# Performance work log

Hardware: AMD Instinct MI355X
Metric: run time of the kernel (lower is better)

Reference implementation:

```python
import jax, jax.numpy as jnp
import numpy as np

B, T, N, C, H, K = 32, 12, 512, 2, 64, 3
P = C + H  # 66, GCN input feature dim


def _xavier(key, fan_in, fan_out):
    std = (2.0 / (fan_in + fan_out)) ** 0.5
    return jax.random.normal(key, (fan_in, fan_out), dtype=jnp.float32) * std


def setup_inputs() -> dict:
    key = jax.random.key(0)
    k1, k2, k3, k4 = jax.random.split(key, 4)
    # scale adjacency so K-hop aggregation stays O(1) in magnitude
    G = jax.random.normal(k1, (K, N, N), dtype=jnp.float32) * (1.0 / np.sqrt(N))
    x_seq = jax.random.normal(k2, (B, T, N, C), dtype=jnp.float32)
    init_h = jnp.zeros((B, N, H), dtype=jnp.float32)
    W_gate = _xavier(k3, K * P, 2 * H)
    b_gate = jnp.zeros((2 * H,), dtype=jnp.float32)
    W_update = _xavier(k4, K * P, H)
    b_update = jnp.zeros((H,), dtype=jnp.float32)
    return {"G": G, "x_seq": x_seq, "init_h": init_h,
            "W_gate": W_gate, "b_gate": b_gate,
            "W_update": W_update, "b_update": b_update}


def _gcn(G, x, W, b):
    # x: [B, N, P]; G: [K, N, N] -> support_cat: [B, N, K*P] (k-major, matching torch cat order)
    Bq, Nq, Pq = x.shape
    sup = jnp.einsum('kij,bjp->bikp', G, x).reshape(Bq, Nq, -1)
    return sup @ W + b


def _cell(G, x, h, Wg, bg, Wu, bu):
    combined = jnp.concatenate([x, h], axis=-1)             # [B,N,C+H]
    zr = jax.nn.sigmoid(_gcn(G, combined, Wg, bg))           # [B,N,2H]
    z, r = zr[..., :H], zr[..., H:]
    candidate = jnp.concatenate([x, r * h], axis=-1)
    hc = jnp.tanh(_gcn(G, candidate, Wu, bu))
    return (1.0 - z) * h + z * hc


def reference(G, x_seq, init_h, W_gate, b_gate, W_update, b_update):
    # scan over time (sequential GRU state dependency)
    xs = jnp.swapaxes(x_seq, 0, 1)  # [T,B,N,C]

    def step(h, x_t):
        h2 = _cell(G, x_t, h, W_gate, b_gate, W_update, b_update)
        return h2, None

    h_last, _ = jax.lax.scan(step, init_h, xs)
    return h_last  # [B,N,H] — last hidden state of the (single) layer
```

## Files before the change

kernel.cpp:

```cpp
#include <hip/hip_runtime.h>
#include <hip/hip_bf16.h>
#include <cmath>

#define NN 512
#define BB 32
#define HH 64
#define TT 12
#define KS 3

#define OFF_GHI   0
#define OFF_GPK   786432
#define OFF_XTH   1572864
#define OFF_SX    1966080
#define OFF_HHI   3145728
#define OFF_HLO   3670016
#define OFF_RHHI  4194304
#define OFF_Z     4718592
#define OFF_WHGH  6291456
#define OFF_WHGL  6304256
#define OFF_WHUH  6317056
#define OFF_WHUL  6323456
#define OFF_WXG   6329856
#define OFF_WXU   6330624

typedef __attribute__((ext_vector_type(8))) short v8s;
typedef __attribute__((ext_vector_type(4))) float f32x4;
typedef __attribute__((ext_vector_type(4))) unsigned short u16x4;

__device__ __forceinline__ unsigned short f2bf(float f) {
  union { __hip_bfloat16 h; unsigned short u; } x;
  x.h = __float2bfloat16(f);
  return x.u;
}
__device__ __forceinline__ float bf2f(unsigned short u) {
  union { unsigned short u; __hip_bfloat16 h; } x;
  x.u = u;
  return __bfloat162float(x.h);
}

__device__ __forceinline__ int swz64(int j, int key) {
  return (j & ~63) | ((((j >> 3) & 7) ^ key) << 3) | (j & 7);
}

__device__ __forceinline__ void gl_lds16(const unsigned short* g, short* l) {
  __builtin_amdgcn_global_load_lds(
      (const __attribute__((address_space(1))) void*)g,
      (__attribute__((address_space(3))) void*)l, 16, 0, 0);
}

__device__ __forceinline__ float fast_tanh(float x) {
  float e = __expf(2.f * x);
  return 1.f - 2.f / (e + 1.f);
}

__global__ __launch_bounds__(256) void prep_all(
    const float* __restrict__ G, const float* __restrict__ x_seq,
    const float* __restrict__ init_h, const float* __restrict__ Wg,
    const float* __restrict__ Wu,
    unsigned short* __restrict__ Ghi, unsigned short* __restrict__ Gpk,
    unsigned short* __restrict__ Xh,
    unsigned short* __restrict__ Hhi, unsigned short* __restrict__ Hlo,
    unsigned short* __restrict__ Whgh, unsigned short* __restrict__ Whgl,
    unsigned short* __restrict__ Whuh, unsigned short* __restrict__ Whul,
    float* __restrict__ Wxg, float* __restrict__ Wxu) {
  int idx = blockIdx.x * 256 + threadIdx.x;
  if (idx < 786432) {
    int j = idx & 511;
    int i = (idx >> 9) & 511;
    Ghi[(size_t)(idx >> 9) * 512 + swz64(j, i & 7)] = f2bf(G[idx]);
  } else if (idx < 884736) {
    int t = idx - 786432;
    int L = t & 63;
    int frag = t >> 6;
    int m = frag % 3;
    int kf = (frag / 3) & 1;
    int j0 = (frag / 6) & 7;
    int i0w = frag / 48;
    int w = i0w & 3, i0 = i0w >> 2;
    int R = w * 48 + m * 16 + (L & 15);
    int ksec = R >> 6;
    int i = i0 * 64 + (R & 63);
    int jb = j0 * 64 + kf * 32 + (L >> 4) * 8;
    unsigned short* dst = Gpk + (size_t)frag * 512 + L * 8;
#pragma unroll
    for (int e = 0; e < 8; ++e) dst[e] = f2bf(G[((size_t)ksec * NN + i) * NN + jb + e]);
  } else if (idx < 1277952) {
    int t2 = idx - 884736;
    int j = t2 & 511;
    int col = t2 >> 9;
    int t = col >> 6;
    int b = (col & 63) >> 1;
    int c = col & 1;
    float v = x_seq[((size_t)(b * TT + t) * NN + j) * 2 + c];
    Xh[(size_t)col * 512 + swz64(j, col & 7)] = f2bf(v);
  } else if (idx < 2326528) {
    int t2 = idx - 1277952;
    int i = t2 & 511;
    int col = t2 >> 9;
    int b = col >> 6;
    int p = col & 63;
    float h = init_h[((size_t)b * NN + i) * HH + p];
    unsigned short hi = f2bf(h);
    size_t pos = (size_t)col * 512 + swz64(i, col & 7);
    Hhi[pos] = hi;
    Hlo[pos] = f2bf(h - bf2f(hi));
  } else if (idx < 2364544) {
    int j2 = idx - 2326528;
    if (j2 < 24576) {
      int o = j2 & 127, kq = j2 >> 7;
      int k = kq >> 6, q = kq & 63;
      float v = Wg[(size_t)(k * 66 + 2 + q) * 128 + o];
      unsigned short hi = f2bf(v);
      Whgh[o * 200 + kq] = hi;
      Whgl[o * 200 + kq] = f2bf(v - bf2f(hi));
    } else if (j2 < 36864) {
      int j = j2 - 24576;
      int o = j & 63, kq = j >> 6;
      int k = kq >> 6, q = kq & 63;
      float v = Wu[(size_t)(k * 66 + 2 + q) * 64 + o];
      unsigned short hi = f2bf(v);
      Whuh[o * 200 + kq] = hi;
      Whul[o * 200 + kq] = f2bf(v - bf2f(hi));
    } else if (j2 < 37632) {
      int j = j2 - 36864;
      int o = j & 127, kc = j >> 7;
      Wxg[kc * 128 + o] = Wg[(size_t)((kc >> 1) * 66 + (kc & 1)) * 128 + o];
    } else {
      int j = j2 - 37632;
      int o = j & 63, kc = j >> 6;
      Wxu[kc * 64 + o] = Wu[(size_t)((kc >> 1) * 66 + (kc & 1)) * 64 + o];
    }
  }
}

__global__ __launch_bounds__(256) void gemm_sx(const unsigned short* __restrict__ Ghi,
                                               const unsigned short* __restrict__ Xh,
                                               float* __restrict__ Sx2) {
  __shared__ __align__(16) short sA[64 * 64];
  __shared__ __align__(16) short sB[64 * 64];
  int tid = threadIdx.x;
  int L = tid & 63, w = tid >> 6;
  int wm = (w >> 1) * 32, wn = (w & 1) * 32;
  int i0 = blockIdx.y * 64;
  int c0 = blockIdx.x * 64;
  f32x4 acc[2][2];
#pragma unroll
  for (int m = 0; m < 2; ++m)
#pragma unroll
    for (int n = 0; n < 2; ++n) acc[m][n] = (f32x4)(0.f);

  for (int j0 = 0; j0 < 512; j0 += 64) {
    __syncthreads();
#pragma unroll
    for (int u = 0; u < 2; ++u) {
      int r = w * 16 + u * 8;
      gl_lds16(Ghi + (size_t)(i0 + r + (L >> 3)) * 512 + j0 + (L & 7) * 8, sA + r * 64);
      gl_lds16(Xh + (size_t)(c0 + r + (L >> 3)) * 512 + j0 + (L & 7) * 8, sB + r * 64);
    }
    __syncthreads();
#pragma unroll
    for (int kf = 0; kf < 2; ++kf) {
      int kog = kf * 4 + (L >> 4);
      v8s af[2], bf[2];
#pragma unroll
      for (int m = 0; m < 2; ++m) {
        int row = wm + m * 16 + (L & 15);
        af[m] = *(const v8s*)(sA + row * 64 + ((kog ^ (row & 7)) << 3));
      }
#pragma unroll
      for (int n = 0; n < 2; ++n) {
        int row = wn + n * 16 + (L & 15);
        bf[n] = *(const v8s*)(sB + row * 64 + ((kog ^ (row & 7)) << 3));
      }
#pragma unroll
      for (int m = 0; m < 2; ++m)
#pragma unroll
        for (int n = 0; n < 2; ++n)
          acc[m][n] = __builtin_amdgcn_mfma_f32_16x16x32_bf16(af[m], bf[n], acc[m][n], 0, 0, 0);
    }
  }
#pragma unroll
  for (int m = 0; m < 2; ++m)
#pragma unroll
    for (int r = 0; r < 4; ++r)
#pragma unroll
      for (int n = 0; n < 2; ++n)
        Sx2[(size_t)(i0 + wm + m * 16 + (L >> 4) * 4 + r) * 768 + c0 + wn + n * 16 + (L & 15)] =
            acc[m][n][r];
}

template <int GATE>
__global__ __launch_bounds__(512, 2) void fused_step(
    const unsigned short* __restrict__ Gpk,
    const unsigned short* __restrict__ Bhi,
    const float* __restrict__ Sx2,
    const unsigned short* __restrict__ Whi,
    const unsigned short* __restrict__ Wlo,
    const float* __restrict__ Wx,
    const float* __restrict__ bias,
    const unsigned short* __restrict__ Hr_hi,
    const unsigned short* __restrict__ Hr_lo,
    unsigned short* __restrict__ Ohi,
    unsigned short* __restrict__ Olo,
    unsigned short* __restrict__ Z,
    float* __restrict__ out, int t) {
  constexpr int O = GATE ? 128 : 64;
  constexpr int NF = GATE ? 4 : 2;
  __shared__ __align__(16) char smem[67584];
  short* sBh = (short*)smem;
  short* sS  = (short*)smem;
  float* sSx = (float*)(smem + 65536);

  int tid = threadIdx.x;
  int L = tid & 63, w = tid >> 6;
  int wm = w & 3, wn = w >> 2;
  int bid = blockIdx.x;
  int c = bid & 7, local = bid >> 3;
  int p = c >> 1, hc = c & 1;
  int b = p * 8 + (local >> 2);
  int i0t = hc * 4 + (local & 3);
  int i0 = i0t * 64;
  int bcol = b * 64;
  const unsigned short* Ap = Gpk + (size_t)(i0t * 4 + wm) * 48 * 512;

#pragma unroll
  for (int u = 0; u < 8; ++u) {
    int col = w * 8 + u;
    gl_lds16(Bhi + (size_t)(bcol + col) * 512 + L * 8, sBh + col * 512);
  }
  for (int e = tid; e < 384; e += 512) {
    int il = e / 6, kc = e % 6;
    sSx[e] = Sx2[(size_t)((kc >> 1) * 512 + i0 + il) * 768 + t * 64 + b * 2 + (kc & 1)];
  }
  __syncthreads();

  f32x4 acc[3][2];
#pragma unroll
  for (int m = 0; m < 3; ++m)
#pragma unroll
    for (int n = 0; n < 2; ++n) acc[m][n] = (f32x4)(0.f);
#pragma unroll
  for (int it = 0; it < 8; ++it) {
    v8s ah[2][3];
#pragma unroll
    for (int kf = 0; kf < 2; ++kf)
#pragma unroll
      for (int m = 0; m < 3; ++m)
        ah[kf][m] = *(const v8s*)(Ap + (size_t)((it * 2 + kf) * 3 + m) * 512 + L * 8);
#pragma unroll
    for (int kf = 0; kf < 2; ++kf) {
      int jj = it * 64 + kf * 32 + (L >> 4) * 8;
      v8s bh[2];
#pragma unroll
      for (int n = 0; n < 2; ++n) {
        int col = wn * 32 + n * 16 + (L & 15);
        int off = col * 512 + ((jj & ~63) | (((((jj >> 3) & 7) ^ (col & 7))) << 3));
        bh[n] = *(const v8s*)(sBh + off);
      }
#pragma unroll
      for (int m = 0; m < 3; ++m)
#pragma unroll
        for (int n = 0; n < 2; ++n)
          acc[m][n] = __builtin_amdgcn_mfma_f32_16x16x32_bf16(ah[kf][m], bh[n], acc[m][n], 0, 0, 0);
    }
  }
  __syncthreads();

#pragma unroll
  for (int m = 0; m < 3; ++m)
#pragma unroll
    for (int n = 0; n < 2; ++n)
#pragma unroll
      for (int r = 0; r < 4; ++r) {
        int R = wm * 48 + m * 16 + (L >> 4) * 4 + r;
        int il = R & 63, kk = R >> 6;
        int pp = wn * 32 + n * 16 + (L & 15);
        float v = acc[m][n][r];
        unsigned short hi = f2bf(v);
        sS[il * 408 + kk * 64 + pp] = (short)hi;
        sS[il * 408 + 200 + kk * 64 + pp] = (short)f2bf(v - bf2f(hi));
      }
  __syncthreads();

  int me = w & 3, oh = w >> 2;
  f32x4 acc2[NF];
#pragma unroll
  for (int n = 0; n < NF; ++n) acc2[n] = (f32x4)(0.f);
#pragma unroll
  for (int s = 0; s < 3; ++s) {
    const unsigned short* Wsrc = (s < 2) ? Whi : Wlo;
    int abase = (s == 1) ? 200 : 0;
#pragma unroll
    for (int f = 0; f < 6; ++f) {
      int k0 = f * 32 + (L >> 4) * 8;
      v8s af2 = *(const v8s*)(sS + (me * 16 + (L & 15)) * 408 + abase + k0);
#pragma unroll
      for (int n = 0; n < NF; ++n) {
        v8s bf2 = *(const v8s*)(Wsrc + (size_t)(oh * (O / 2) + n * 16 + (L & 15)) * 200 + k0);
        acc2[n] = __builtin_amdgcn_mfma_f32_16x16x32_bf16(af2, bf2, acc2[n], 0, 0, 0);
      }
    }
  }

#pragma unroll
  for (int n = 0; n < NF; ++n) {
    int o = oh * (O / 2) + n * 16 + (L & 15);
    int il0 = me * 16 + (L >> 4) * 4;
    float vals[4];
#pragma unroll
    for (int r = 0; r < 4; ++r) {
      float v = acc2[n][r] + bias[o];
#pragma unroll
      for (int kc = 0; kc < 6; ++kc) v += sSx[(il0 + r) * 6 + kc] * Wx[kc * O + o];
      vals[r] = v;
    }
    if (GATE) {
      float sg[4];
#pragma unroll
      for (int r = 0; r < 4; ++r) sg[r] = 1.f / (1.f + __expf(-vals[r]));
      if (oh == 0) {
#pragma unroll
        for (int r = 0; r < 4; ++r)
          Z[((size_t)b * 512 + i0 + il0 + r) * 64 + o] = f2bf(sg[r]);
      } else {
        int col = bcol + (o - 64);
        size_t cb = (size_t)col * 512 + i0 + (((il0 >> 3) ^ (col & 7)) << 3) + (il0 & 7);
        u16x4 h4 = *(const u16x4*)(Hr_hi + cb);
        u16x4 l4 = *(const u16x4*)(Hr_lo + cb);
        u16x4 oh4;
#pragma unroll
        for (int r = 0; r < 4; ++r) {
          float h = bf2f(h4[r]) + bf2f(l4[r]);
          oh4[r] = f2bf(sg[r] * h);
        }
        *(u16x4*)(Ohi + cb) = oh4;
      }
    } else {
      int col = bcol + o;
      size_t cb = (size_t)col * 512 + i0 + (((il0 >> 3) ^ (col & 7)) << 3) + (il0 & 7);
      u16x4 h4 = *(const u16x4*)(Hr_hi + cb);
      u16x4 l4 = *(const u16x4*)(Hr_lo + cb);
      u16x4 oh4, ol4;
#pragma unroll
      for (int r = 0; r < 4; ++r) {
        float hc2 = fast_tanh(vals[r]);
        float z = bf2f(Z[((size_t)b * 512 + i0 + il0 + r) * 64 + o]);
        float h = bf2f(h4[r]) + bf2f(l4[r]);
        float hn = (1.f - z) * h + z * hc2;
        unsigned short hi = f2bf(hn);
        oh4[r] = hi;
        ol4[r] = f2bf(hn - bf2f(hi));
        if (t == TT - 1) out[((size_t)b * 512 + i0 + il0 + r) * 64 + o] = hn;
      }
      *(u16x4*)(Ohi + cb) = oh4;
      *(u16x4*)(Olo + cb) = ol4;
    }
  }
}

extern "C" void kernel_launch(void* const* d_in, const int* in_sizes, int n_in,
                              void* d_out, int out_size, void* d_ws, size_t ws_size,
                              hipStream_t stream) {
  const float* G      = (const float*)d_in[0];
  const float* x_seq  = (const float*)d_in[1];
  const float* init_h = (const float*)d_in[2];
  const float* Wg     = (const float*)d_in[3];
  const float* bg     = (const float*)d_in[4];
  const float* Wu     = (const float*)d_in[5];
  const float* bu     = (const float*)d_in[6];
  float* out = (float*)d_out;
  float* ws = (float*)d_ws;

  unsigned short* GHI  = (unsigned short*)(ws + OFF_GHI);
  unsigned short* GPK  = (unsigned short*)(ws + OFF_GPK);
  unsigned short* Xh   = (unsigned short*)(ws + OFF_XTH);
  float* Sx2           = ws + OFF_SX;
  unsigned short* Hhi  = (unsigned short*)(ws + OFF_HHI);
  unsigned short* Hlo  = (unsigned short*)(ws + OFF_HLO);
  unsigned short* RHhi = (unsigned short*)(ws + OFF_RHHI);
  unsigned short* Z    = (unsigned short*)(ws + OFF_Z);
  unsigned short* Whgh = (unsigned short*)(ws + OFF_WHGH);
  unsigned short* Whgl = (unsigned short*)(ws + OFF_WHGL);
  unsigned short* Whuh = (unsigned short*)(ws + OFF_WHUH);
  unsigned short* Whul = (unsigned short*)(ws + OFF_WHUL);
  float* Wxg           = ws + OFF_WXG;
  float* Wxu           = ws + OFF_WXU;

  prep_all<<<9237, 256, 0, stream>>>(G, x_seq, init_h, Wg, Wu, GHI, GPK, Xh,
                                     Hhi, Hlo, Whgh, Whgl, Whuh, Whul, Wxg, Wxu);
  gemm_sx<<<dim3(12, 24), 256, 0, stream>>>(GHI, Xh, Sx2);

  for (int t = 0; t < TT; ++t) {
    fused_step<1><<<256, 512, 0, stream>>>(GPK, Hhi, Sx2, Whgh, Whgl, Wxg, bg,
                                           Hhi, Hlo, RHhi, RHhi, Z, out, t);
    fused_step<0><<<256, 512, 0, stream>>>(GPK, RHhi, Sx2, Whuh, Whul, Wxu, bu,
                                           Hhi, Hlo, Hhi, Hlo, Z, out, t);
  }
}
```

Measured before the change: 361.4 us.

## Replace per-step kernel launches with persistent kernel using per-batch group barriers

The 24 per-timestep launches of the gate and update kernels become one persistent kernel. Each block claims a slot on its own XCC via an atomic counter, so the 8 blocks of a batch share an XCC and synchronize through a lightweight per-batch group barrier instead of kernel boundaries. The z gate is kept in shared memory rather than round-tripped through global memory. This removes launch overhead and global Z traffic, but it relies on all 256 blocks being co-resident and on exactly 32 blocks landing on each XCC. The spin barrier has a timeout break, so a scheduling mismatch could give silently wrong results instead of a hang.

Result: slower. 1.263 ms (+249.6%).

```diff
diff --git a/kernel.cpp b/kernel.cpp
--- a/kernel.cpp
+++ b/kernel.cpp
@@ -15,7 +15,7 @@
 #define OFF_HHI   3145728
 #define OFF_HLO   3670016
 #define OFF_RHHI  4194304
-#define OFF_Z     4718592
+#define OFF_BAR   4718592
 #define OFF_WHGH  6291456
 #define OFF_WHGL  6304256
 #define OFF_WHUH  6317056
@@ -189,171 +189,230 @@
             acc[m][n][r];
 }
 
-template <int GATE>
-__global__ __launch_bounds__(512, 2) void fused_step(
+__device__ __forceinline__ void groupbar(unsigned int* gb) {
+  __syncthreads();
+  if (threadIdx.x == 0) {
+    __builtin_amdgcn_fence(__ATOMIC_RELEASE, "agent");
+    unsigned int g = __hip_atomic_load(gb + 1, __ATOMIC_RELAXED, __HIP_MEMORY_SCOPE_AGENT);
+    unsigned int old =
+        __hip_atomic_fetch_add(gb, 1u, __ATOMIC_RELEASE, __HIP_MEMORY_SCOPE_AGENT);
+    if (old == 7u) {
+      __hip_atomic_store(gb, 0u, __ATOMIC_RELAXED, __HIP_MEMORY_SCOPE_AGENT);
+      __hip_atomic_store(gb + 1, g + 1u, __ATOMIC_RELEASE, __HIP_MEMORY_SCOPE_AGENT);
+    } else {
+      int sp = 0;
+      while (__hip_atomic_load(gb + 1, __ATOMIC_ACQUIRE, __HIP_MEMORY_SCOPE_AGENT) == g) {
+        __builtin_amdgcn_s_sleep(2);
+        if (++sp > (1 << 24)) break;
+      }
+    }
+    __builtin_amdgcn_fence(__ATOMIC_ACQUIRE, "agent");
+  }
+  __syncthreads();
+}
+
+__global__ __launch_bounds__(512, 2) void persist(
     const unsigned short* __restrict__ Gpk,
-    const unsigned short* __restrict__ Bhi,
+    unsigned short* __restrict__ Hhi, unsigned short* __restrict__ Hlo,
+    unsigned short* __restrict__ RHhi,
     const float* __restrict__ Sx2,
-    const unsigned short* __restrict__ Whi,
-    const unsigned short* __restrict__ Wlo,
-    const float* __restrict__ Wx,
-    const float* __restrict__ bias,
-    const unsigned short* __restrict__ Hr_hi,
-    const unsigned short* __restrict__ Hr_lo,
-    unsigned short* __restrict__ Ohi,
-    unsigned short* __restrict__ Olo,
-    unsigned short* __restrict__ Z,
-    float* __restrict__ out, int t) {
-  constexpr int O = GATE ? 128 : 64;
-  constexpr int NF = GATE ? 4 : 2;
-  __shared__ __align__(16) char smem[67584];
+    const unsigned short* __restrict__ Whgh, const unsigned short* __restrict__ Whgl,
+    const float* __restrict__ Wxg, const float* __restrict__ bg,
+    const unsigned short* __restrict__ Whuh, const unsigned short* __restrict__ Whul,
+    const float* __restrict__ Wxu, const float* __restrict__ bu,
+    float* __restrict__ out, unsigned int* __restrict__ bar) {
+  __shared__ __align__(16) char smem[83456];
+  __shared__ unsigned int sSlot;
   short* sBh = (short*)smem;
   short* sS  = (short*)smem;
   float* sSx = (float*)(smem + 65536);
+  float* sZ  = (float*)(smem + 67072);
 
   int tid = threadIdx.x;
   int L = tid & 63, w = tid >> 6;
   int wm = w & 3, wn = w >> 2;
-  int bid = blockIdx.x;
-  int c = bid & 7, local = bid >> 3;
-  int p = c >> 1, hc = c & 1;
-  int b = p * 8 + (local >> 2);
-  int i0t = hc * 4 + (local & 3);
+
+  unsigned int xcc;
+  asm volatile("s_getreg_b32 %0, hwreg(HW_REG_XCC_ID)" : "=s"(xcc));
+  xcc &= 7u;
+  if (tid == 0) {
+    unsigned int s =
+        __hip_atomic_fetch_add(bar + xcc, 1u, __ATOMIC_RELAXED, __HIP_MEMORY_SCOPE_AGENT) & 31u;
+    sSlot = xcc * 32u + s;
+  }
+  __syncthreads();
+  unsigned int slot = sSlot;
+  int b = (int)(slot >> 3);
+  int i0t = (int)(slot & 7u);
   int i0 = i0t * 64;
   int bcol = b * 64;
+  unsigned int* gb = bar + 8 + b * 2;
   const unsigned short* Ap = Gpk + (size_t)(i0t * 4 + wm) * 48 * 512;
 
-#pragma unroll
-  for (int u = 0; u < 8; ++u) {
-    int col = w * 8 + u;
-    gl_lds16(Bhi + (size_t)(bcol + col) * 512 + L * 8, sBh + col * 512);
-  }
-  for (int e = tid; e < 384; e += 512) {
-    int il = e / 6, kc = e % 6;
-    sSx[e] = Sx2[(size_t)((kc >> 1) * 512 + i0 + il) * 768 + t * 64 + b * 2 + (kc & 1)];
-  }
-  __syncthreads();
-
-  f32x4 acc[3][2];
-#pragma unroll
-  for (int m = 0; m < 3; ++m)
-#pragma unroll
-    for (int n = 0; n < 2; ++n) acc[m][n] = (f32x4)(0.f);
-#pragma unroll
-  for (int it = 0; it < 8; ++it) {
-    v8s ah[2][3];
-#pragma unroll
-    for (int kf = 0; kf < 2; ++kf)
+  for (int t = 0; t < TT; ++t) {
+#pragma unroll 1
+    for (int ph = 0; ph < 2; ++ph) {
+      const int GATE = (ph == 0);
+      const unsigned short* Bsrc = GATE ? Hhi : RHhi;
+
+#pragma unroll
+      for (int u = 0; u < 8; ++u) {
+        int col = w * 8 + u;
+        gl_lds16(Bsrc + (size_t)(bcol + col) * 512 + L * 8, sBh + col * 512);
+      }
+      if (GATE) {
+        for (int e = tid; e < 384; e += 512) {
+          int il = e / 6, kc = e % 6;
+          sSx[e] = Sx2[(size_t)((kc >> 1) * 512 + i0 + il) * 768 + t * 64 + b * 2 + (kc & 1)];
+        }
+      }
+      __syncthreads();
+
+      f32x4 acc[3][2];
 #pragma unroll
       for (int m = 0; m < 3; ++m)
-        ah[kf][m] = *(const v8s*)(Ap + (size_t)((it * 2 + kf) * 3 + m) * 512 + L * 8);
-#pragma unroll
-    for (int kf = 0; kf < 2; ++kf) {
-      int jj = it * 64 + kf * 32 + (L >> 4) * 8;
-      v8s bh[2];
-#pragma unroll
-      for (int n = 0; n < 2; ++n) {
-        int col = wn * 32 + n * 16 + (L & 15);
-        int off = col * 512 + ((jj & ~63) | (((((jj >> 3) & 7) ^ (col & 7))) << 3));
-        bh[n] = *(const v8s*)(sBh + off);
-      }
+#pragma unroll
+        for (int n = 0; n < 2; ++n) acc[m][n] = (f32x4)(0.f);
+#pragma unroll
+      for (int it = 0; it < 8; ++it) {
+        v8s ah[2][3];
+#pragma unroll
+        for (int kf = 0; kf < 2; ++kf)
+#pragma unroll
+          for (int m = 0; m < 3; ++m)
+            ah[kf][m] = *(const v8s*)(Ap + (size_t)((it * 2 + kf) * 3 + m) * 512 + L * 8);
+#pragma unroll
+        for (int kf = 0; kf < 2; ++kf) {
+          int jj = it * 64 + kf * 32 + (L >> 4) * 8;
+          v8s bh[2];
+#pragma unroll
+          for (int n = 0; n < 2; ++n) {
+            int col = wn * 32 + n * 16 + (L & 15);
+            int off = col * 512 + ((jj & ~63) | (((((jj >> 3) & 7) ^ (col & 7))) << 3));
+            bh[n] = *(const v8s*)(sBh + off);
+          }
+#pragma unroll
+          for (int m = 0; m < 3; ++m)
+#pragma unroll
+            for (int n = 0; n < 2; ++n)
+              acc[m][n] =
+                  __builtin_amdgcn_mfma_f32_16x16x32_bf16(ah[kf][m], bh[n], acc[m][n], 0, 0, 0);
+        }
+      }
+      __syncthreads();
+
 #pragma unroll
       for (int m = 0; m < 3; ++m)
 #pragma unroll
         for (int n = 0; n < 2; ++n)
-          acc[m][n] = __builtin_amdgcn_mfma_f32_16x16x32_bf16(ah[kf][m], bh[n], acc[m][n], 0, 0, 0);
-    }
-  }
-  __syncthreads();
-
-#pragma unroll
-  for (int m = 0; m < 3; ++m)
-#pragma unroll
-    for (int n = 0; n < 2; ++n)
-#pragma unroll
-      for (int r = 0; r < 4; ++r) {
-        int R = wm * 48 + m * 16 + (L >> 4) * 4 + r;
-        int il = R & 63, kk = R >> 6;
-        int pp = wn * 32 + n * 16 + (L & 15);
-        float v = acc[m][n][r];
-        unsigned short hi = f2bf(v);
-        sS[il * 408 + kk * 64 + pp] = (short)hi;
-        sS[il * 408 + 200 + kk * 64 + pp] = (short)f2bf(v - bf2f(hi));
-      }
-  __syncthreads();
-
-  int me = w & 3, oh = w >> 2;
-  f32x4 acc2[NF];
-#pragma unroll
-  for (int n = 0; n < NF; ++n) acc2[n] = (f32x4)(0.f);
-#pragma unroll
-  for (int s = 0; s < 3; ++s) {
-    const unsigned short* Wsrc = (s < 2) ? Whi : Wlo;
-    int abase = (s == 1) ? 200 : 0;
-#pragma unroll
-    for (int f = 0; f < 6; ++f) {
-      int k0 = f * 32 + (L >> 4) * 8;
-      v8s af2 = *(const v8s*)(sS + (me * 16 + (L & 15)) * 408 + abase + k0);
-#pragma unroll
-      for (int n = 0; n < NF; ++n) {
-        v8s bf2 = *(const v8s*)(Wsrc + (size_t)(oh * (O / 2) + n * 16 + (L & 15)) * 200 + k0);
-        acc2[n] = __builtin_amdgcn_mfma_f32_16x16x32_bf16(af2, bf2, acc2[n], 0, 0, 0);
-      }
-    }
-  }
-
-#pragma unroll
-  for (int n = 0; n < NF; ++n) {
-    int o = oh * (O / 2) + n * 16 + (L & 15);
-    int il0 = me * 16 + (L >> 4) * 4;
-    float vals[4];
-#pragma unroll
-    for (int r = 0; r < 4; ++r) {
-      float v = acc2[n][r] + bias[o];
-#pragma unroll
-      for (int kc = 0; kc < 6; ++kc) v += sSx[(il0 + r) * 6 + kc] * Wx[kc * O + o];
-      vals[r] = v;
-    }
-    if (GATE) {
-      float sg[4];
-#pragma unroll
-      for (int r = 0; r < 4; ++r) sg[r] = 1.f / (1.f + __expf(-vals[r]));
-      if (oh == 0) {
-#pragma unroll
-        for (int r = 0; r < 4; ++r)
-          Z[((size_t)b * 512 + i0 + il0 + r) * 64 + o] = f2bf(sg[r]);
+#pragma unroll
+          for (int r = 0; r < 4; ++r) {
+            int R = wm * 48 + m * 16 + (L >> 4) * 4 + r;
+            int il = R & 63, kk = R >> 6;
+            int pp = wn * 32 + n * 16 + (L & 15);
+            float v = acc[m][n][r];
+            unsigned short hi = f2bf(v);
+            sS[il * 408 + kk * 64 + pp] = (short)hi;
+            sS[il * 408 + 200 + kk * 64 + pp] = (short)f2bf(v - bf2f(hi));
+          }
+      __syncthreads();
+
+      int me = w & 3, oh = w >> 2;
+      if (GATE) {
+        f32x4 acc2[4];
+#pragma unroll
+        for (int n = 0; n < 4; ++n) acc2[n] = (f32x4)(0.f);
+#pragma unroll
+        for (int s = 0; s < 3; ++s) {
+          const unsigned short* Wsrc = (s < 2) ? Whgh : Whgl;
+          int abase = (s == 1) ? 200 : 0;
+#pragma unroll
+          for (int f = 0; f < 6; ++f) {
+            int k0 = f * 32 + (L >> 4) * 8;
+            v8s af2 = *(const v8s*)(sS + (me * 16 + (L & 15)) * 408 + abase + k0);
+#pragma unroll
+            for (int n = 0; n < 4; ++n) {
+              v8s bf2 = *(const v8s*)(Wsrc + (size_t)(oh * 64 + n * 16 + (L & 15)) * 200 + k0);
+              acc2[n] = __builtin_amdgcn_mfma_f32_16x16x32_bf16(af2, bf2, acc2[n], 0, 0, 0);
+            }
+          }
+        }
+#pragma unroll
+        for (int n = 0; n < 4; ++n) {
+          int o = oh * 64 + n * 16 + (L & 15);
+          int il0 = me * 16 + (L >> 4) * 4;
+          float sg[4];
+#pragma unroll
+          for (int r = 0; r < 4; ++r) {
+            float v = acc2[n][r] + bg[o];
+#pragma unroll
+            for (int kc = 0; kc < 6; ++kc) v += sSx[(il0 + r) * 6 + kc] * Wxg[kc * 128 + o];
+            sg[r] = 1.f / (1.f + __expf(-v));
+          }
+          if (oh == 0) {
+#pragma unroll
+            for (int r = 0; r < 4; ++r) sZ[(il0 + r) * 64 + o] = sg[r];
+          } else {
+            int col = bcol + (o - 64);
+            size_t cb = (size_t)col * 512 + i0 + (((il0 >> 3) ^ (col & 7)) << 3) + (il0 & 7);
+            u16x4 h4 = *(const u16x4*)(Hhi + cb);
+            u16x4 l4 = *(const u16x4*)(Hlo + cb);
+            u16x4 oh4;
+#pragma unroll
+            for (int r = 0; r < 4; ++r) {
+              float h = bf2f(h4[r]) + bf2f(l4[r]);
+              oh4[r] = f2bf(sg[r] * h);
+            }
+            *(u16x4*)(RHhi + cb) = oh4;
+          }
+        }
       } else {
-        int col = bcol + (o - 64);
-        size_t cb = (size_t)col * 512 + i0 + (((il0 >> 3) ^ (col & 7)) << 3) + (il0 & 7);
-        u16x4 h4 = *(const u16x4*)(Hr_hi + cb);
-        u16x4 l4 = *(const u16x4*)(Hr_lo + cb);
-        u16x4 oh4;
-#pragma unroll
-        for (int r = 0; r < 4; ++r) {
-          float h = bf2f(h4[r]) + bf2f(l4[r]);
-          oh4[r] = f2bf(sg[r] * h);
-        }
-        *(u16x4*)(Ohi + cb) = oh4;
-      }
-    } else {
-      int col = bcol + o;
-      size_t cb = (size_t)col * 512 + i0 + (((il0 >> 3) ^ (col & 7)) << 3) + (il0 & 7);
-      u16x4 h4 = *(const u16x4*)(Hr_hi + cb);
-      u16x4 l4 = *(const u16x4*)(Hr_lo + cb);
-      u16x4 oh4, ol4;
-#pragma unroll
-      for (int r = 0; r < 4; ++r) {
-        float hc2 = fast_tanh(vals[r]);
-        float z = bf2f(Z[((size_t)b * 512 + i0 + il0 + r) * 64 + o]);
-        float h = bf2f(h4[r]) + bf2f(l4[r]);
-        float hn = (1.f - z) * h + z * hc2;
-        unsigned short hi = f2bf(hn);
-        oh4[r] = hi;
-        ol4[r] = f2bf(hn - bf2f(hi));
-        if (t == TT - 1) out[((size_t)b * 512 + i0 + il0 + r) * 64 + o] = hn;
-      }
-      *(u16x4*)(Ohi + cb) = oh4;
-      *(u16x4*)(Olo + cb) = ol4;
+        f32x4 acc2[2];
+#pragma unroll
+        for (int n = 0; n < 2; ++n) acc2[n] = (f32x4)(0.f);
+#pragma unroll
+        for (int s = 0; s < 3; ++s) {
+          const unsigned short* Wsrc = (s < 2) ? Whuh : Whul;
+          int abase = (s == 1) ? 200 : 0;
+#pragma unroll
+          for (int f = 0; f < 6; ++f) {
+            int k0 = f * 32 + (L >> 4) * 8;
+            v8s af2 = *(const v8s*)(sS + (me * 16 + (L & 15)) * 408 + abase + k0);
+#pragma unroll
+            for (int n = 0; n < 2; ++n) {
+              v8s bf2 = *(const v8s*)(Wsrc + (size_t)(oh * 32 + n * 16 + (L & 15)) * 200 + k0);
+              acc2[n] = __builtin_amdgcn_mfma_f32_16x16x32_bf16(af2, bf2, acc2[n], 0, 0, 0);
+            }
+          }
+        }
+#pragma unroll
+        for (int n = 0; n < 2; ++n) {
+          int o = oh * 32 + n * 16 + (L & 15);
+          int il0 = me * 16 + (L >> 4) * 4;
+          int col = bcol + o;
+          size_t cb = (size_t)col * 512 + i0 + (((il0 >> 3) ^ (col & 7)) << 3) + (il0 & 7);
+          u16x4 h4 = *(const u16x4*)(Hhi + cb);
+          u16x4 l4 = *(const u16x4*)(Hlo + cb);
+          u16x4 oh4, ol4;
+#pragma unroll
+          for (int r = 0; r < 4; ++r) {
+            float v = acc2[n][r] + bu[o];
+#pragma unroll
+            for (int kc = 0; kc < 6; ++kc) v += sSx[(il0 + r) * 6 + kc] * Wxu[kc * 64 + o];
+            float hc2 = fast_tanh(v);
+            float z = sZ[(il0 + r) * 64 + o];
+            float h = bf2f(h4[r]) + bf2f(l4[r]);
+            float hn = (1.f - z) * h + z * hc2;
+            unsigned short hi = f2bf(hn);
+            oh4[r] = hi;
+            ol4[r] = f2bf(hn - bf2f(hi));
+            if (t == TT - 1) out[((size_t)b * 512 + i0 + il0 + r) * 64 + o] = hn;
+          }
+          *(u16x4*)(Hhi + cb) = oh4;
+          *(u16x4*)(Hlo + cb) = ol4;
+        }
+      }
+      if (t != TT - 1 || ph != 1) groupbar(gb);
     }
   }
 }
@@ -378,7 +437,7 @@
   unsigned short* Hhi  = (unsigned short*)(ws + OFF_HHI);
   unsigned short* Hlo  = (unsigned short*)(ws + OFF_HLO);
   unsigned short* RHhi = (unsigned short*)(ws + OFF_RHHI);
-  unsigned short* Z    = (unsigned short*)(ws + OFF_Z);
+  unsigned int* bar    = (unsigned int*)(ws + OFF_BAR);
   unsigned short* Whgh = (unsigned short*)(ws + OFF_WHGH);
   unsigned short* Whgl = (unsigned short*)(ws + OFF_WHGL);
   unsigned short* Whuh = (unsigned short*)(ws + OFF_WHUH);
@@ -386,14 +445,11 @@
   float* Wxg           = ws + OFF_WXG;
   float* Wxu           = ws + OFF_WXU;
 
+  (void)hipMemsetAsync(bar, 0, (8 + 64) * 4, stream);
   prep_all<<<9237, 256, 0, stream>>>(G, x_seq, init_h, Wg, Wu, GHI, GPK, Xh,
                                      Hhi, Hlo, Whgh, Whgl, Whuh, Whul, Wxg, Wxu);
   gemm_sx<<<dim3(12, 24), 256, 0, stream>>>(GHI, Xh, Sx2);
 
-  for (int t = 0; t < TT; ++t) {
-    fused_step<1><<<256, 512, 0, stream>>>(GPK, Hhi, Sx2, Whgh, Whgl, Wxg, bg,
-                                           Hhi, Hlo, RHhi, RHhi, Z, out, t);
-    fused_step<0><<<256, 512, 0, stream>>>(GPK, RHhi, Sx2, Whuh, Whul, Wxu, bu,
-                                           Hhi, Hlo, Hhi, Hlo, Z, out, t);
-  }
-}
+  persist<<<256, 512, 0, stream>>>(GPK, Hhi, Hlo, RHhi, Sx2,
+                                   Whgh, Whgl, Wxg, bg, Whuh, Whul, Wxu, bu, out, bar);
+}
```
